# Kernel optimization log

Measured on AMD Instinct MI355X. Metric: run time of the kernel, lower is better.

Reference implementation:

```python
import jax, jax.numpy as jnp
import numpy as np

B, F, T = 4, 2048, 2048
CF, CT = 1024, 1024
H, DH = 16, 64
ALPHA = 1.0 / np.sqrt(DH).astype(np.float32)


def setup_inputs() -> dict:
    key = jax.random.key(0)
    ks = jax.random.split(key, 8)
    s = 0.02  # trunc_normal-ish init scale
    return {
        "from_tensor": jax.random.normal(ks[0], (B, F, CF), jnp.float32),
        "to_tensor": jax.random.normal(ks[1], (B, T, CT), jnp.float32),
        "mask": jax.random.randint(ks[2], (B, F, T), 0, 2, jnp.int32),
        "Wq": jax.random.normal(ks[3], (CF, H * DH), jnp.float32) * s,
        "bq": jnp.zeros((H * DH,), jnp.float32),
        "Wk": jax.random.normal(ks[4], (CT, H * DH), jnp.float32) * s,
        "bk": jnp.zeros((H * DH,), jnp.float32),
        "Wv": jax.random.normal(ks[5], (CT, H * DH), jnp.float32) * s,
        "bv": jnp.zeros((H * DH,), jnp.float32),
    }


def reference(from_tensor, to_tensor, mask, Wq, bq, Wk, bk, Wv, bv):
    # projections (nn.Linear with no activation)
    q = from_tensor @ Wq + bq          # [B,F,H*DH]
    k = to_tensor @ Wk + bk            # [B,T,H*DH]
    v = to_tensor @ Wv + bv            # [B,T,H*DH]
    q = q.reshape(B, F, H, DH)         # query: [..., F, H, DH]
    k = k.reshape(B, T, DH, H)         # key:   [..., T, DH, H]  (self._shape[::-1])
    v = v.reshape(B, T, H, DH)
    # score = transpose(q,-3,-2) @ transpose(k,-3,-1) * alpha -> [B,H,F,T]
    score = jnp.einsum("bfhd,btdh->bhft", q, k) * ALPHA
    if mask is not None:
        adder = (1.0 - mask[:, None].astype(score.dtype)) * -100000.0  # [B,1,F,T]
        score = score + adder
    probs = jax.nn.softmax(score, axis=-1)  # dropout p=0.0 -> identity
    # context = probs @ transpose(v,-3,-2), then transpose back: [B,F,H,DH]
    context = jnp.einsum("bhft,bthd->bfhd", probs, v)
    return context.reshape(B, F, H * DH)
```

## Files before the change

kernel.cpp:

```cpp
#include <hip/hip_runtime.h>
#include <type_traits>

typedef __bf16 bf16_t;
typedef __attribute__((ext_vector_type(8))) __bf16 bf16x8;
typedef __attribute__((ext_vector_type(4))) float f32x4;
typedef __attribute__((ext_vector_type(16))) float f32x16;

__device__ __forceinline__ void async16(const void* g, void* lds) {
  __builtin_amdgcn_global_load_lds((const __attribute__((address_space(1))) unsigned int*)g,
                                   (__attribute__((address_space(3))) unsigned int*)lds, 16, 0, 0);
}

__device__ __forceinline__ unsigned pk2(float lo, float hi) {
  unsigned short a = __builtin_bit_cast(unsigned short, (__bf16)lo);
  unsigned short b = __builtin_bit_cast(unsigned short, (__bf16)hi);
  return (unsigned)a | ((unsigned)b << 16);
}

__device__ __forceinline__ void plswap(unsigned& a, unsigned& b) {
#if __has_builtin(__builtin_amdgcn_permlane32_swap)
  auto r = __builtin_amdgcn_permlane32_swap((int)a, (int)b, false, false);
  a = (unsigned)r[0];
  b = (unsigned)r[1];
#else
  const bool hb = (threadIdx.x & 32) != 0;
  unsigned bx = (unsigned)__shfl_xor((int)b, 32);
  unsigned ax = (unsigned)__shfl_xor((int)a, 32);
  unsigned na = hb ? bx : a;
  unsigned nb = hb ? b : ax;
  a = na; b = nb;
#endif
}

__global__ __launch_bounds__(256) void pack_mask_kernel(const int* __restrict__ mask,
                                                        unsigned long long* __restrict__ mb) {
  const int lane = threadIdx.x & 63, w = threadIdx.x >> 6;
  for (int i = 0; i < 32; ++i) {
    size_t word = (size_t)blockIdx.x * 128 + (size_t)i * 4 + w;
    unsigned long long bits = __ballot(mask[word * 64 + lane] != 0);
    if (lane == 0) mb[word] = bits;
  }
}

__global__ __launch_bounds__(256) void cvt_bf16_kernel(const float* __restrict__ in, bf16_t* __restrict__ out) {
  size_t i = (size_t)blockIdx.x * 256 + threadIdx.x;
  const float4* in4 = (const float4*)in;
  float4 a = in4[i * 2], b = in4[i * 2 + 1];
  bf16x8 o;
  o[0] = (__bf16)a.x; o[1] = (__bf16)a.y; o[2] = (__bf16)a.z; o[3] = (__bf16)a.w;
  o[4] = (__bf16)b.x; o[5] = (__bf16)b.y; o[6] = (__bf16)b.z; o[7] = (__bf16)b.w;
  *(bf16x8*)(out + i * 8) = o;
}

__global__ __launch_bounds__(256) void wt_cvt_kernel(const float* __restrict__ Wq, const float* __restrict__ Wk,
                                                     const float* __restrict__ Wv, bf16_t* __restrict__ Wt) {
  const int z = blockIdx.z;
  const float* src = (z == 0) ? Wq : ((z == 1) ? Wk : Wv);
  const float sc = (z == 0) ? 0.18033688011112042f : 1.0f;
  bf16_t* dst = Wt + (size_t)z * 1024 * 1024;
  const int n = blockIdx.x * 64 + (threadIdx.x & 63);
  const int k8 = blockIdx.y * 4 + (threadIdx.x >> 6);
  bf16x8 o;
#pragma unroll
  for (int j = 0; j < 8; ++j) o[j] = (__bf16)(src[(size_t)(k8 * 8 + j) * 1024 + n] * sc);
  *(bf16x8*)(dst + (size_t)n * 1024 + k8 * 8) = o;
}

__global__ __launch_bounds__(256) void proj_kernel(const bf16_t* __restrict__ A, const bf16_t* __restrict__ Wt,
                                                   const float* __restrict__ bias, bf16_t* __restrict__ dst,
                                                   const int z, const float bscale) {
  __shared__ __align__(16) unsigned char smem[33792];
  bf16_t* se = (bf16_t*)smem;
  const int tid = threadIdx.x, lane = tid & 63, w = tid >> 6;
  const int m0 = blockIdx.x * 128, n0 = blockIdx.y * 128;
  const int wm = (w >> 1) * 64, wn = (w & 1) * 64;
  const int r = lane & 15, kq = lane >> 4;
  const int srow = lane >> 2, sslot = lane & 3;
  f32x4 acc[4][4] = {};

  auto stage = [&](int buf, int k0) {
    bf16_t* Ad = se + buf * 4096;
    bf16_t* Bd = se + 8192 + buf * 4096;
#pragma unroll
    for (int it = 0; it < 2; ++it) {
      const int c = it * 4 + w;
      const int row = c * 16 + srow;
      async16(A + (size_t)(m0 + row) * 1024 + k0 + ((sslot ^ (row & 3)) * 8), Ad + c * 512);
      async16(Wt + (size_t)(n0 + row) * 1024 + k0 + ((sslot ^ (row & 3)) * 8), Bd + c * 512);
    }
  };

  stage(0, 0);
  __syncthreads();
  for (int tile = 0; tile < 32; ++tile) {
    const int cur = tile & 1;
    if (tile < 31) stage(cur ^ 1, (tile + 1) * 32);
    const bf16_t* Al = se + cur * 4096;
    const bf16_t* Bl = se + 8192 + cur * 4096;
    bf16x8 af[4], bfr[4];
#pragma unroll
    for (int i = 0; i < 4; ++i) {
      const int ra = wm + i * 16 + r;
      af[i] = *(const bf16x8*)(Al + ra * 32 + ((kq ^ (ra & 3)) * 8));
      const int rb = wn + i * 16 + r;
      bfr[i] = *(const bf16x8*)(Bl + rb * 32 + ((kq ^ (rb & 3)) * 8));
    }
    __builtin_amdgcn_s_setprio(1);
#pragma unroll
    for (int i = 0; i < 4; ++i)
#pragma unroll
      for (int j = 0; j < 4; ++j)
        acc[i][j] = __builtin_amdgcn_mfma_f32_16x16x32_bf16(af[i], bfr[j], acc[i][j], 0, 0, 0);
    __builtin_amdgcn_s_setprio(0);
    __syncthreads();
  }

  bf16_t* Cl = se;
  float bvv[4];
#pragma unroll
  for (int j = 0; j < 4; ++j) bvv[j] = bias[n0 + wn + j * 16 + r] * bscale;
#pragma unroll
  for (int i = 0; i < 4; ++i)
#pragma unroll
    for (int j = 0; j < 4; ++j)
#pragma unroll
      for (int g = 0; g < 4; ++g)
        Cl[(wm + i * 16 + kq * 4 + g) * 132 + wn + j * 16 + r] = (__bf16)(acc[i][j][g] + bvv[j]);
  __syncthreads();

  const int b = m0 >> 11, sbase = m0 & 2047;
  if (z == 0) {
#pragma unroll
    for (int q = 0; q < 8; ++q) {
      const int cid = q * 256 + tid;
      const int m = cid >> 4, c = (cid >> 3) & 1, d8 = cid & 7;
      bf16x8 val = *(const bf16x8*)(Cl + m * 132 + c * 64 + d8 * 8);
      *(bf16x8*)(dst + ((size_t)(b * 16 + (n0 >> 6) + c) * 2048 + sbase + m) * 64 + d8 * 8) = val;
    }
  } else if (z == 1) {
#pragma unroll
    for (int q = 0; q < 8; ++q) {
      const int cid = q * 256 + tid;
      const int hh = cid >> 7, m = cid & 127;
      bf16x8 val;
#pragma unroll
      for (int dd = 0; dd < 8; ++dd) val[dd] = Cl[m * 132 + dd * 16 + hh];
      *(bf16x8*)(dst + ((size_t)(b * 16 + hh) * 2048 + sbase + m) * 64 + (n0 >> 4)) = val;
    }
  } else {
#pragma unroll
    for (int q = 0; q < 8; ++q) {
      const int cid = q * 256 + tid;
      const int nl = cid >> 4, m8 = cid & 15;
      bf16x8 val;
#pragma unroll
      for (int s = 0; s < 8; ++s) val[s] = Cl[(m8 * 8 + s) * 132 + nl];
      const int hh = (n0 >> 6) + (nl >> 6), dd = nl & 63;
      *(bf16x8*)(dst + ((size_t)(b * 16 + hh) * 64 + dd) * 2048 + sbase + m8 * 8) = val;
    }
  }
}

__global__ __launch_bounds__(256, 2) void attn_kernel(const bf16_t* __restrict__ Q, const bf16_t* __restrict__ K,
                                                      const bf16_t* __restrict__ VT,
                                                      const unsigned long long* __restrict__ mb,
                                                      float* __restrict__ out) {
  __shared__ __align__(16) unsigned char smem[32768];
  bf16_t* se = (bf16_t*)smem;
  const int tid = threadIdx.x, lane = tid & 63, w = tid >> 6;
  const int cl = lane & 31, hi = lane >> 5;
  const int f0 = blockIdx.x * 256, h = blockIdx.y, b = blockIdx.z;
  const size_t bh = (size_t)b * 16 + h;
  const int fw = f0 + w * 64;

  const bf16_t* Qb = Q + (bh * 2048 + fw) * 64;
  bf16x8 qf[2][4];
#pragma unroll
  for (int fb = 0; fb < 2; ++fb)
#pragma unroll
    for (int ks = 0; ks < 4; ++ks)
      qf[fb][ks] = *(const bf16x8*)(Qb + (fb * 32 + cl) * 64 + ks * 16 + hi * 8);

  f32x16 Of[2][2] = {};
  float lacc[2] = {0.f, 0.f};

  const unsigned long long* mrow[2];
  mrow[0] = mb + ((size_t)b * 2048 + fw + cl) * 32;
  mrow[1] = mb + ((size_t)b * 2048 + fw + 32 + cl) * 32;

  auto stage = [&](int buf, int t0) {
    bf16_t* Kd = se + buf * 4096;
    bf16_t* Vd = se + 8192 + buf * 4096;
    const int row8 = lane >> 3, slot = lane & 7;
#pragma unroll
    for (int it = 0; it < 2; ++it) {
      const int c = it * 4 + w;
      const int row = c * 8 + row8;
      async16(K + (bh * 2048 + t0 + row) * 64 + ((slot ^ (row & 7)) * 8), Kd + c * 512);
      async16(VT + (bh * 64 + row) * 2048 + t0 + ((slot ^ (row & 7)) * 8), Vd + c * 512);
    }
  };

  unsigned long long mA[2], mB[2];
  auto mload = [&](unsigned long long (&m)[2], int tileIdx) {
    m[0] = mrow[0][tileIdx];
    m[1] = mrow[1][tileIdx];
  };

  stage(0, 0);
  mload(mA, 0);
  __syncthreads();

  auto body = [&](auto curc, unsigned long long (&mc)[2], unsigned long long (&mn)[2], int tile) {
    constexpr int cur = decltype(curc)::value;
    if (tile < 31) {
      stage(cur ^ 1, (tile + 1) * 64);
      mload(mn, tile + 1);
    }
    const bf16_t* Kl = se + cur * 4096;
    const bf16_t* Vl = se + 8192 + cur * 4096;

    unsigned paw[2][4][4];

#pragma unroll
    for (int ts = 0; ts < 2; ++ts) {
      f32x16 stf[2] = {};
      const int krow = ts * 32 + cl;
      __builtin_amdgcn_s_setprio(1);
#pragma unroll
      for (int ks = 0; ks < 4; ++ks) {
        bf16x8 kf = *(const bf16x8*)(Kl + krow * 64 + (((2 * ks + hi) ^ (krow & 7)) * 8));
        stf[0] = __builtin_amdgcn_mfma_f32_32x32x16_bf16(kf, qf[0][ks], stf[0], 0, 0, 0);
        stf[1] = __builtin_amdgcn_mfma_f32_32x32x16_bf16(kf, qf[1][ks], stf[1], 0, 0, 0);
      }
      __builtin_amdgcn_s_setprio(0);

#pragma unroll
      for (int fb = 0; fb < 2; ++fb) {
        const unsigned mword = (unsigned)(mc[fb] >> (ts * 32 + 4 * hi));
        float pv[16];
#pragma unroll
        for (int q = 0; q < 4; ++q)
#pragma unroll
          for (int e = 0; e < 4; ++e) {
            const int idx = q * 4 + e;
            float p = __builtin_amdgcn_exp2f(stf[fb][idx]);
            p = ((mword >> (e + 8 * q)) & 1u) ? p : 0.f;
            lacc[fb] += p;
            pv[idx] = p;
          }
#pragma unroll
        for (int kl = 0; kl < 2; ++kl) {
          const int qa = 2 * kl, qb = qa + 1;
          unsigned x0 = pk2(pv[qa * 4 + 0], pv[qa * 4 + 1]);
          unsigned y0 = pk2(pv[qb * 4 + 0], pv[qb * 4 + 1]);
          unsigned x1 = pk2(pv[qa * 4 + 2], pv[qa * 4 + 3]);
          unsigned y1 = pk2(pv[qb * 4 + 2], pv[qb * 4 + 3]);
          plswap(x0, y0);
          plswap(x1, y1);
          paw[fb][ts * 2 + kl][0] = x0;
          paw[fb][ts * 2 + kl][1] = x1;
          paw[fb][ts * 2 + kl][2] = y0;
          paw[fb][ts * 2 + kl][3] = y1;
        }
      }
    }

    union PW { unsigned w[4]; bf16x8 v; };
    __builtin_amdgcn_s_setprio(1);
#pragma unroll
    for (int db = 0; db < 2; ++db) {
      const int vrow0 = db * 32 + cl;
#pragma unroll
      for (int kt = 0; kt < 4; ++kt) {
        bf16x8 vf = *(const bf16x8*)(Vl + vrow0 * 64 + (((2 * kt + hi) ^ (vrow0 & 7)) * 8));
        PW a0, a1;
#pragma unroll
        for (int ww = 0; ww < 4; ++ww) { a0.w[ww] = paw[0][kt][ww]; a1.w[ww] = paw[1][kt][ww]; }
        Of[0][db] = __builtin_amdgcn_mfma_f32_32x32x16_bf16(a0.v, vf, Of[0][db], 0, 0, 0);
        Of[1][db] = __builtin_amdgcn_mfma_f32_32x32x16_bf16(a1.v, vf, Of[1][db], 0, 0, 0);
      }
    }
    __builtin_amdgcn_s_setprio(0);
    __syncthreads();
  };

  for (int tile = 0; tile < 32; tile += 2) {
    body(std::integral_constant<int, 0>{}, mA, mB, tile);
    body(std::integral_constant<int, 1>{}, mB, mA, tile + 1);
  }

#pragma unroll
  for (int fb = 0; fb < 2; ++fb) lacc[fb] += __shfl_xor(lacc[fb], 32);
  float* lsh = (float*)smem;
  if (hi == 0) {
    lsh[w * 64 + cl] = lacc[0];
    lsh[w * 64 + 32 + cl] = lacc[1];
  }
#pragma unroll
  for (int fb = 0; fb < 2; ++fb)
#pragma unroll
    for (int q = 0; q < 4; ++q)
#pragma unroll
      for (int e = 0; e < 4; ++e) {
        const int idx = q * 4 + e;
        const int row = e + 8 * q + 4 * hi;
        const float li = 1.0f / lsh[w * 64 + fb * 32 + row];
        const size_t orow = ((size_t)b * 2048 + fw + fb * 32 + row) * 1024 + h * 64;
        out[orow + cl] = Of[fb][0][idx] * li;
        out[orow + 32 + cl] = Of[fb][1][idx] * li;
      }
}

extern "C" void kernel_launch(void* const* d_in, const int* in_sizes, int n_in,
                              void* d_out, int out_size, void* d_ws, size_t ws_size,
                              hipStream_t stream) {
  (void)in_sizes; (void)n_in; (void)out_size; (void)ws_size;
  const float* from = (const float*)d_in[0];
  const float* to_  = (const float*)d_in[1];
  const int*   mask = (const int*)d_in[2];
  const float* Wq = (const float*)d_in[3];
  const float* bq = (const float*)d_in[4];
  const float* Wk = (const float*)d_in[5];
  const float* bk = (const float*)d_in[6];
  const float* Wv = (const float*)d_in[7];
  const float* bv = (const float*)d_in[8];
  float* out = (float*)d_out;
  char* ws = (char*)d_ws;

  bf16_t* Qw = (bf16_t*)(ws);
  bf16_t* Kw = (bf16_t*)(ws + (size_t)(1u << 24));
  bf16_t* Vw = (bf16_t*)(ws + (size_t)(2u << 24));
  bf16_t* Wt = (bf16_t*)(ws + (size_t)(3u << 24));
  unsigned long long* mbits = (unsigned long long*)(ws + (size_t)(3u << 24) + (size_t)(6u << 20));
  bf16_t* inb = (bf16_t*)(ws + (size_t)(3u << 24) + (size_t)(8u << 20));

  pack_mask_kernel<<<2048, 256, 0, stream>>>(mask, mbits);
  wt_cvt_kernel<<<dim3(16, 32, 3), 256, 0, stream>>>(Wq, Wk, Wv, Wt);
  cvt_bf16_kernel<<<4096, 256, 0, stream>>>(from, inb);
  proj_kernel<<<dim3(64, 8), 256, 0, stream>>>(inb, Wt, bq, Qw, 0, 0.18033688011112042f);
  cvt_bf16_kernel<<<4096, 256, 0, stream>>>(to_, inb);
  proj_kernel<<<dim3(64, 8), 256, 0, stream>>>(inb, Wt + (1u << 20), bk, Kw, 1, 1.0f);
  proj_kernel<<<dim3(64, 8), 256, 0, stream>>>(inb, Wt + (2u << 20), bv, Vw, 2, 1.0f);
  attn_kernel<<<dim3(8, 16, 4), 256, 0, stream>>>(Qw, Kw, Vw, mbits, out);
}
```

Before: 225.8 us.

## Halve query rows per wave in attention to raise occupancy

Each wave now processes 32 query rows instead of 64, so a block covers 128 rows and the grid doubles to 1024 blocks. This halves the per-wave accumulator and score registers, allowing launch bounds of 4 blocks per SIMD group. The cost is that each K/V tile loaded into LDS is reused across half as many query rows, doubling total K/V and mask traffic, and each K fragment read now feeds one MFMA instead of two. A __syncthreads is also added before the row-sum read from shared memory.

```diff
diff --git a/kernel.cpp b/kernel.cpp
--- a/kernel.cpp
+++ b/kernel.cpp
@@ -161,7 +161,7 @@
   }
 }
 
-__global__ __launch_bounds__(256, 2) void attn_kernel(const bf16_t* __restrict__ Q, const bf16_t* __restrict__ K,
+__global__ __launch_bounds__(256, 4) void attn_kernel(const bf16_t* __restrict__ Q, const bf16_t* __restrict__ K,
                                                       const bf16_t* __restrict__ VT,
                                                       const unsigned long long* __restrict__ mb,
                                                       float* __restrict__ out) {
@@ -169,24 +169,20 @@
   bf16_t* se = (bf16_t*)smem;
   const int tid = threadIdx.x, lane = tid & 63, w = tid >> 6;
   const int cl = lane & 31, hi = lane >> 5;
-  const int f0 = blockIdx.x * 256, h = blockIdx.y, b = blockIdx.z;
+  const int f0 = blockIdx.x * 128, h = blockIdx.y, b = blockIdx.z;
   const size_t bh = (size_t)b * 16 + h;
-  const int fw = f0 + w * 64;
+  const int fw = f0 + w * 32;
 
   const bf16_t* Qb = Q + (bh * 2048 + fw) * 64;
-  bf16x8 qf[2][4];
-#pragma unroll
-  for (int fb = 0; fb < 2; ++fb)
-#pragma unroll
-    for (int ks = 0; ks < 4; ++ks)
-      qf[fb][ks] = *(const bf16x8*)(Qb + (fb * 32 + cl) * 64 + ks * 16 + hi * 8);
-
-  f32x16 Of[2][2] = {};
-  float lacc[2] = {0.f, 0.f};
-
-  const unsigned long long* mrow[2];
-  mrow[0] = mb + ((size_t)b * 2048 + fw + cl) * 32;
-  mrow[1] = mb + ((size_t)b * 2048 + fw + 32 + cl) * 32;
+  bf16x8 qf[4];
+#pragma unroll
+  for (int ks = 0; ks < 4; ++ks)
+    qf[ks] = *(const bf16x8*)(Qb + cl * 64 + ks * 16 + hi * 8);
+
+  f32x16 Of[2] = {};
+  float lacc = 0.f;
+
+  const unsigned long long* mrow = mb + ((size_t)b * 2048 + fw + cl) * 32;
 
   auto stage = [&](int buf, int t0) {
     bf16_t* Kd = se + buf * 4096;
@@ -201,68 +197,59 @@
     }
   };
 
-  unsigned long long mA[2], mB[2];
-  auto mload = [&](unsigned long long (&m)[2], int tileIdx) {
-    m[0] = mrow[0][tileIdx];
-    m[1] = mrow[1][tileIdx];
-  };
-
+  unsigned long long mA, mB;
   stage(0, 0);
-  mload(mA, 0);
+  mA = mrow[0];
   __syncthreads();
 
-  auto body = [&](auto curc, unsigned long long (&mc)[2], unsigned long long (&mn)[2], int tile) {
+  auto body = [&](auto curc, unsigned long long& mc, unsigned long long& mn, int tile) {
     constexpr int cur = decltype(curc)::value;
     if (tile < 31) {
       stage(cur ^ 1, (tile + 1) * 64);
-      mload(mn, tile + 1);
+      mn = mrow[tile + 1];
     }
     const bf16_t* Kl = se + cur * 4096;
     const bf16_t* Vl = se + 8192 + cur * 4096;
 
-    unsigned paw[2][4][4];
+    unsigned paw[4][4];
 
 #pragma unroll
     for (int ts = 0; ts < 2; ++ts) {
-      f32x16 stf[2] = {};
+      f32x16 stf = {};
       const int krow = ts * 32 + cl;
       __builtin_amdgcn_s_setprio(1);
 #pragma unroll
       for (int ks = 0; ks < 4; ++ks) {
         bf16x8 kf = *(const bf16x8*)(Kl + krow * 64 + (((2 * ks + hi) ^ (krow & 7)) * 8));
-        stf[0] = __builtin_amdgcn_mfma_f32_32x32x16_bf16(kf, qf[0][ks], stf[0], 0, 0, 0);
-        stf[1] = __builtin_amdgcn_mfma_f32_32x32x16_bf16(kf, qf[1][ks], stf[1], 0, 0, 0);
+        stf = __builtin_amdgcn_mfma_f32_32x32x16_bf16(kf, qf[ks], stf, 0, 0, 0);
       }
       __builtin_amdgcn_s_setprio(0);
 
-#pragma unroll
-      for (int fb = 0; fb < 2; ++fb) {
-        const unsigned mword = (unsigned)(mc[fb] >> (ts * 32 + 4 * hi));
-        float pv[16];
-#pragma unroll
-        for (int q = 0; q < 4; ++q)
-#pragma unroll
-          for (int e = 0; e < 4; ++e) {
-            const int idx = q * 4 + e;
-            float p = __builtin_amdgcn_exp2f(stf[fb][idx]);
-            p = ((mword >> (e + 8 * q)) & 1u) ? p : 0.f;
-            lacc[fb] += p;
-            pv[idx] = p;
-          }
-#pragma unroll
-        for (int kl = 0; kl < 2; ++kl) {
-          const int qa = 2 * kl, qb = qa + 1;
-          unsigned x0 = pk2(pv[qa * 4 + 0], pv[qa * 4 + 1]);
-          unsigned y0 = pk2(pv[qb * 4 + 0], pv[qb * 4 + 1]);
-          unsigned x1 = pk2(pv[qa * 4 + 2], pv[qa * 4 + 3]);
-          unsigned y1 = pk2(pv[qb * 4 + 2], pv[qb * 4 + 3]);
-          plswap(x0, y0);
-          plswap(x1, y1);
-          paw[fb][ts * 2 + kl][0] = x0;
-          paw[fb][ts * 2 + kl][1] = x1;
-          paw[fb][ts * 2 + kl][2] = y0;
-          paw[fb][ts * 2 + kl][3] = y1;
+      const unsigned mword = (unsigned)(mc >> (ts * 32 + 4 * hi));
+      float pv[16];
+#pragma unroll
+      for (int q = 0; q < 4; ++q)
+#pragma unroll
+        for (int e = 0; e < 4; ++e) {
+          const int idx = q * 4 + e;
+          float p = __builtin_amdgcn_exp2f(stf[idx]);
+          p = ((mword >> (e + 8 * q)) & 1u) ? p : 0.f;
+          lacc += p;
+          pv[idx] = p;
         }
+#pragma unroll
+      for (int kl = 0; kl < 2; ++kl) {
+        const int qa = 2 * kl, qb = qa + 1;
+        unsigned x0 = pk2(pv[qa * 4 + 0], pv[qa * 4 + 1]);
+        unsigned y0 = pk2(pv[qb * 4 + 0], pv[qb * 4 + 1]);
+        unsigned x1 = pk2(pv[qa * 4 + 2], pv[qa * 4 + 3]);
+        unsigned y1 = pk2(pv[qb * 4 + 2], pv[qb * 4 + 3]);
+        plswap(x0, y0);
+        plswap(x1, y1);
+        paw[ts * 2 + kl][0] = x0;
+        paw[ts * 2 + kl][1] = x1;
+        paw[ts * 2 + kl][2] = y0;
+        paw[ts * 2 + kl][3] = y1;
       }
     }
 
@@ -274,11 +261,10 @@
 #pragma unroll
       for (int kt = 0; kt < 4; ++kt) {
         bf16x8 vf = *(const bf16x8*)(Vl + vrow0 * 64 + (((2 * kt + hi) ^ (vrow0 & 7)) * 8));
-        PW a0, a1;
-#pragma unroll
-        for (int ww = 0; ww < 4; ++ww) { a0.w[ww] = paw[0][kt][ww]; a1.w[ww] = paw[1][kt][ww]; }
-        Of[0][db] = __builtin_amdgcn_mfma_f32_32x32x16_bf16(a0.v, vf, Of[0][db], 0, 0, 0);
-        Of[1][db] = __builtin_amdgcn_mfma_f32_32x32x16_bf16(a1.v, vf, Of[1][db], 0, 0, 0);
+        PW a0;
+#pragma unroll
+        for (int ww = 0; ww < 4; ++ww) a0.w[ww] = paw[kt][ww];
+        Of[db] = __builtin_amdgcn_mfma_f32_32x32x16_bf16(a0.v, vf, Of[db], 0, 0, 0);
       }
     }
     __builtin_amdgcn_s_setprio(0);
@@ -290,26 +276,21 @@
     body(std::integral_constant<int, 1>{}, mB, mA, tile + 1);
   }
 
-#pragma unroll
-  for (int fb = 0; fb < 2; ++fb) lacc[fb] += __shfl_xor(lacc[fb], 32);
+  lacc += __shfl_xor(lacc, 32);
   float* lsh = (float*)smem;
-  if (hi == 0) {
-    lsh[w * 64 + cl] = lacc[0];
-    lsh[w * 64 + 32 + cl] = lacc[1];
-  }
-#pragma unroll
-  for (int fb = 0; fb < 2; ++fb)
-#pragma unroll
-    for (int q = 0; q < 4; ++q)
-#pragma unroll
-      for (int e = 0; e < 4; ++e) {
-        const int idx = q * 4 + e;
-        const int row = e + 8 * q + 4 * hi;
-        const float li = 1.0f / lsh[w * 64 + fb * 32 + row];
-        const size_t orow = ((size_t)b * 2048 + fw + fb * 32 + row) * 1024 + h * 64;
-        out[orow + cl] = Of[fb][0][idx] * li;
-        out[orow + 32 + cl] = Of[fb][1][idx] * li;
-      }
+  if (hi == 0) lsh[w * 32 + cl] = lacc;
+  __syncthreads();
+#pragma unroll
+  for (int q = 0; q < 4; ++q)
+#pragma unroll
+    for (int e = 0; e < 4; ++e) {
+      const int idx = q * 4 + e;
+      const int row = e + 8 * q + 4 * hi;
+      const float li = 1.0f / lsh[w * 32 + row];
+      const size_t orow = ((size_t)b * 2048 + fw + row) * 1024 + h * 64;
+      out[orow + cl] = Of[0][idx] * li;
+      out[orow + 32 + cl] = Of[1][idx] * li;
+    }
 }
 
 extern "C" void kernel_launch(void* const* d_in, const int* in_sizes, int n_in,
@@ -342,5 +323,5 @@
   cvt_bf16_kernel<<<4096, 256, 0, stream>>>(to_, inb);
   proj_kernel<<<dim3(64, 8), 256, 0, stream>>>(inb, Wt + (1u << 20), bk, Kw, 1, 1.0f);
   proj_kernel<<<dim3(64, 8), 256, 0, stream>>>(inb, Wt + (2u << 20), bv, Vw, 2, 1.0f);
-  attn_kernel<<<dim3(8, 16, 4), 256, 0, stream>>>(Qw, Kw, Vw, mbits, out);
-}
+  attn_kernel<<<dim3(16, 16, 4), 256, 0, stream>>>(Qw, Kw, Vw, mbits, out);
+}
```

After: 239.3 us. +6.0%, slower.

## Software-pipeline PV matmul one tile behind QK and stage V lagged

Applied to the files above, without the earlier changes.

Restructures the attention main loop so the P·V MFMAs for tile i-1 are interleaved between the two halves of the QK^T computation for tile i. V loads are issued one tile later than K loads, and probabilities are kept in registers across iterations. Global address bases are also precomputed once instead of per stage. The goal is to overlap exp/softmax VALU work with matrix-core work and to shorten dependency chains, at the cost of higher register pressure from carrying paw across tiles.

```diff
diff --git a/kernel.cpp b/kernel.cpp
--- a/kernel.cpp
+++ b/kernel.cpp
@@ -183,60 +183,102 @@
 
   f32x16 Of[2][2] = {};
   float lacc[2] = {0.f, 0.f};
+  bf16x8 paw[2][4];
 
   const unsigned long long* mrow[2];
   mrow[0] = mb + ((size_t)b * 2048 + fw + cl) * 32;
   mrow[1] = mb + ((size_t)b * 2048 + fw + 32 + cl) * 32;
 
-  auto stage = [&](int buf, int t0) {
-    bf16_t* Kd = se + buf * 4096;
-    bf16_t* Vd = se + 8192 + buf * 4096;
-    const int row8 = lane >> 3, slot = lane & 7;
-#pragma unroll
-    for (int it = 0; it < 2; ++it) {
-      const int c = it * 4 + w;
-      const int row = c * 8 + row8;
-      async16(K + (bh * 2048 + t0 + row) * 64 + ((slot ^ (row & 7)) * 8), Kd + c * 512);
-      async16(VT + (bh * 64 + row) * 2048 + t0 + ((slot ^ (row & 7)) * 8), Vd + c * 512);
-    }
+  const int row8 = lane >> 3, slot = lane & 7;
+  const int swz = (slot ^ row8) * 8;
+  const bf16_t* kgb[2];
+  const bf16_t* vgb[2];
+#pragma unroll
+  for (int it = 0; it < 2; ++it) {
+    const int row = it * 32 + w * 8 + row8;
+    kgb[it] = K + (bh * 2048 + row) * 64 + swz;
+    vgb[it] = VT + (bh * 64 + row) * 2048 + swz;
+  }
+
+  auto stage_k = [&](int buf, int tile) {
+    bf16_t* kd = se + buf * 4096 + w * 512;
+#pragma unroll
+    for (int it = 0; it < 2; ++it)
+      async16(kgb[it] + (size_t)tile * 4096, kd + it * 2048);
+  };
+  auto stage_v = [&](int buf, int tile) {
+    bf16_t* vd = se + 8192 + buf * 4096 + w * 512;
+#pragma unroll
+    for (int it = 0; it < 2; ++it)
+      async16(vgb[it] + (size_t)tile * 64, vd + it * 2048);
+  };
+
+  auto pv_step = [&](int vbuf) {
+    const bf16_t* Vl = se + 8192 + vbuf * 4096;
+    __builtin_amdgcn_s_setprio(1);
+#pragma unroll
+    for (int db = 0; db < 2; ++db) {
+      const int vrow0 = db * 32 + cl;
+#pragma unroll
+      for (int kt = 0; kt < 4; ++kt) {
+        bf16x8 vf = *(const bf16x8*)(Vl + vrow0 * 64 + (((2 * kt + hi) ^ (vrow0 & 7)) * 8));
+        Of[0][db] = __builtin_amdgcn_mfma_f32_32x32x16_bf16(paw[0][kt], vf, Of[0][db], 0, 0, 0);
+        Of[1][db] = __builtin_amdgcn_mfma_f32_32x32x16_bf16(paw[1][kt], vf, Of[1][db], 0, 0, 0);
+      }
+    }
+    __builtin_amdgcn_s_setprio(0);
   };
 
   unsigned long long mA[2], mB[2];
-  auto mload = [&](unsigned long long (&m)[2], int tileIdx) {
-    m[0] = mrow[0][tileIdx];
-    m[1] = mrow[1][tileIdx];
-  };
-
-  stage(0, 0);
-  mload(mA, 0);
+  stage_k(0, 0);
+  mA[0] = mrow[0][0];
+  mA[1] = mrow[1][0];
   __syncthreads();
 
-  auto body = [&](auto curc, unsigned long long (&mc)[2], unsigned long long (&mn)[2], int tile) {
+  auto body = [&](auto curc, auto dopvc, unsigned long long (&mc)[2], unsigned long long (&mn)[2], int tile) {
     constexpr int cur = decltype(curc)::value;
+    constexpr bool dopv = decltype(dopvc)::value;
     if (tile < 31) {
-      stage(cur ^ 1, (tile + 1) * 64);
-      mload(mn, tile + 1);
-    }
+      stage_k(cur ^ 1, tile + 1);
+      mn[0] = mrow[0][tile + 1];
+      mn[1] = mrow[1][tile + 1];
+    }
+    stage_v(cur, tile);
     const bf16_t* Kl = se + cur * 4096;
-    const bf16_t* Vl = se + 8192 + cur * 4096;
-
-    unsigned paw[2][4][4];
-
-#pragma unroll
-    for (int ts = 0; ts < 2; ++ts) {
-      f32x16 stf[2] = {};
-      const int krow = ts * 32 + cl;
+
+    f32x16 st0[2] = {};
+    {
+      const int krow = cl;
       __builtin_amdgcn_s_setprio(1);
 #pragma unroll
       for (int ks = 0; ks < 4; ++ks) {
         bf16x8 kf = *(const bf16x8*)(Kl + krow * 64 + (((2 * ks + hi) ^ (krow & 7)) * 8));
-        stf[0] = __builtin_amdgcn_mfma_f32_32x32x16_bf16(kf, qf[0][ks], stf[0], 0, 0, 0);
-        stf[1] = __builtin_amdgcn_mfma_f32_32x32x16_bf16(kf, qf[1][ks], stf[1], 0, 0, 0);
+        st0[0] = __builtin_amdgcn_mfma_f32_32x32x16_bf16(kf, qf[0][ks], st0[0], 0, 0, 0);
+        st0[1] = __builtin_amdgcn_mfma_f32_32x32x16_bf16(kf, qf[1][ks], st0[1], 0, 0, 0);
       }
       __builtin_amdgcn_s_setprio(0);
-
+    }
+
+    if constexpr (dopv) pv_step(cur ^ 1);
+
+    f32x16 st1[2] = {};
+    {
+      const int krow = 32 + cl;
+      __builtin_amdgcn_s_setprio(1);
+#pragma unroll
+      for (int ks = 0; ks < 4; ++ks) {
+        bf16x8 kf = *(const bf16x8*)(Kl + krow * 64 + (((2 * ks + hi) ^ (krow & 7)) * 8));
+        st1[0] = __builtin_amdgcn_mfma_f32_32x32x16_bf16(kf, qf[0][ks], st1[0], 0, 0, 0);
+        st1[1] = __builtin_amdgcn_mfma_f32_32x32x16_bf16(kf, qf[1][ks], st1[1], 0, 0, 0);
+      }
+      __builtin_amdgcn_s_setprio(0);
+    }
+
+#pragma unroll
+    for (int ts = 0; ts < 2; ++ts) {
 #pragma unroll
       for (int fb = 0; fb < 2; ++fb) {
+        const f32x16& stf = (ts == 0) ? st0[fb] : st1[fb];
         const unsigned mword = (unsigned)(mc[fb] >> (ts * 32 + 4 * hi));
         float pv[16];
 #pragma unroll
@@ -244,7 +286,7 @@
 #pragma unroll
           for (int e = 0; e < 4; ++e) {
             const int idx = q * 4 + e;
-            float p = __builtin_amdgcn_exp2f(stf[fb][idx]);
+            float p = __builtin_amdgcn_exp2f(stf[idx]);
             p = ((mword >> (e + 8 * q)) & 1u) ? p : 0.f;
             lacc[fb] += p;
             pv[idx] = p;
@@ -258,37 +300,27 @@
           unsigned y1 = pk2(pv[qb * 4 + 2], pv[qb * 4 + 3]);
           plswap(x0, y0);
           plswap(x1, y1);
-          paw[fb][ts * 2 + kl][0] = x0;
-          paw[fb][ts * 2 + kl][1] = x1;
-          paw[fb][ts * 2 + kl][2] = y0;
-          paw[fb][ts * 2 + kl][3] = y1;
+          union { unsigned u[4]; bf16x8 v; } tmp;
+          tmp.u[0] = x0; tmp.u[1] = x1; tmp.u[2] = y0; tmp.u[3] = y1;
+          paw[fb][ts * 2 + kl] = tmp.v;
         }
       }
     }
-
-    union PW { unsigned w[4]; bf16x8 v; };
-    __builtin_amdgcn_s_setprio(1);
-#pragma unroll
-    for (int db = 0; db < 2; ++db) {
-      const int vrow0 = db * 32 + cl;
-#pragma unroll
-      for (int kt = 0; kt < 4; ++kt) {
-        bf16x8 vf = *(const bf16x8*)(Vl + vrow0 * 64 + (((2 * kt + hi) ^ (vrow0 & 7)) * 8));
-        PW a0, a1;
-#pragma unroll
-        for (int ww = 0; ww < 4; ++ww) { a0.w[ww] = paw[0][kt][ww]; a1.w[ww] = paw[1][kt][ww]; }
-        Of[0][db] = __builtin_amdgcn_mfma_f32_32x32x16_bf16(a0.v, vf, Of[0][db], 0, 0, 0);
-        Of[1][db] = __builtin_amdgcn_mfma_f32_32x32x16_bf16(a1.v, vf, Of[1][db], 0, 0, 0);
-      }
-    }
-    __builtin_amdgcn_s_setprio(0);
     __syncthreads();
   };
 
-  for (int tile = 0; tile < 32; tile += 2) {
-    body(std::integral_constant<int, 0>{}, mA, mB, tile);
-    body(std::integral_constant<int, 1>{}, mB, mA, tile + 1);
-  }
+  using c0 = std::integral_constant<int, 0>;
+  using c1 = std::integral_constant<int, 1>;
+  using bF = std::integral_constant<bool, false>;
+  using bT = std::integral_constant<bool, true>;
+
+  body(c0{}, bF{}, mA, mB, 0);
+  body(c1{}, bT{}, mB, mA, 1);
+  for (int tile = 2; tile < 32; tile += 2) {
+    body(c0{}, bT{}, mA, mB, tile);
+    body(c1{}, bT{}, mB, mA, tile + 1);
+  }
+  pv_step(1);
 
 #pragma unroll
   for (int fb = 0; fb < 2; ++fb) lacc[fb] += __shfl_xor(lacc[fb], 32);
```

Result: no change. 225.3 us (-0.2%).
